# Kernel optimization log

Hardware: AMD Instinct MI355X
Metric: run time of the kernel (lower is better)

## Reference

```python
import jax, jax.numpy as jnp
import numpy as np

D_MODEL = 1024
NUM_HEADS = 16
DEPTH = D_MODEL // NUM_HEADS


def setup_inputs() -> dict:
    key = jax.random.key(0)
    ks = jax.random.split(key, 12)
    B, S = 2, 2048
    s = 0.02
    return {
        "q": jax.random.normal(ks[0], (B, S, D_MODEL), dtype=jnp.float32),
        "k": jax.random.normal(ks[1], (B, S, D_MODEL), dtype=jnp.float32),
        "v": jax.random.normal(ks[2], (B, S, D_MODEL), dtype=jnp.float32),
        "mask": jnp.ones((B, 1, 1, S), dtype=bool),  # accepted but unused, as in source
        "wq": jax.random.normal(ks[3], (D_MODEL, D_MODEL), dtype=jnp.float32) * s,
        "bq": jnp.zeros((D_MODEL,), dtype=jnp.float32),
        "wk": jax.random.normal(ks[4], (D_MODEL, D_MODEL), dtype=jnp.float32) * s,
        "bk": jnp.zeros((D_MODEL,), dtype=jnp.float32),
        "wv": jax.random.normal(ks[5], (D_MODEL, D_MODEL), dtype=jnp.float32) * s,
        "bv": jnp.zeros((D_MODEL,), dtype=jnp.float32),
        "wo": jax.random.normal(ks[6], (D_MODEL, D_MODEL), dtype=jnp.float32) * s,
        "bo": jnp.zeros((D_MODEL,), dtype=jnp.float32),
    }


def _split_heads(x, B):
    # [B, S, d_model] -> [B, H, S, depth]
    return x.reshape(B, -1, NUM_HEADS, DEPTH).transpose(0, 2, 1, 3)


def reference(q, k, v, mask, wq, bq, wk, bk, wv, bv, wo, bo):
    B = q.shape[0]
    qh = _split_heads(q @ wq + bq, B)  # [B,H,Sq,depth]
    kh = _split_heads(k @ wk + bk, B)  # [B,H,Sk,depth]
    vh = _split_heads(v @ wv + bv, B)  # [B,H,Sk,depth]
    scale = 1.0 / jnp.sqrt(jnp.asarray(DEPTH, dtype=qh.dtype))
    scores = jnp.einsum("bhqd,bhkd->bhqk", qh, kh) * scale  # [B,H,Sq,Sk]
    attn = jax.nn.softmax(scores, axis=-1)
    ctx = jnp.einsum("bhqk,bhkd->bhqd", attn, vh)  # [B,H,Sq,depth]
    concat = ctx.transpose(0, 2, 1, 3).reshape(B, -1, D_MODEL)  # [B,Sq,d_model]
    out = concat @ wo + bo
    return (out, attn)
```

## Files before the change

kernel.cpp:

```cpp
#include <hip/hip_runtime.h>
#include <hip/hip_bf16.h>
#include <cstdint>
#include <cstddef>

#define BATCH 2
#define SEQ 2048
#define NH 16
#define DH 64
#define DM 1024
#define MTOT 4096

typedef __attribute__((ext_vector_type(8))) short short8;
typedef __attribute__((ext_vector_type(4))) float f32x4;

#define MFMA16(a, b, c) __builtin_amdgcn_mfma_f32_16x16x32_bf16((a), (b), (c), 0, 0, 0)

__device__ __forceinline__ unsigned short f2bf(float f) {
  unsigned int u = __builtin_bit_cast(unsigned int, f);
  u += 0x7fffu + ((u >> 16) & 1u);
  return (unsigned short)(u >> 16);
}

__global__ __launch_bounds__(256) void cvt_x(const float* __restrict__ q,
                                             const float* __restrict__ k,
                                             const float* __restrict__ v,
                                             unsigned short* __restrict__ dst) {
  const float* srcs[3] = {q, k, v};
  const float* s = srcs[blockIdx.y];
  unsigned short* d = dst + (size_t)blockIdx.y * (MTOT * DM);
  int i = blockIdx.x * 256 + threadIdx.x;
  if (i < (MTOT * DM / 4)) {
    float4 f = ((const float4*)s)[i];
    ushort4 o;
    o.x = f2bf(f.x); o.y = f2bf(f.y); o.z = f2bf(f.z); o.w = f2bf(f.w);
    ((ushort4*)d)[i] = o;
  }
}

__global__ __launch_bounds__(256) void cvt_w(const float* __restrict__ w0,
                                             const float* __restrict__ w1,
                                             const float* __restrict__ w2,
                                             const float* __restrict__ w3,
                                             unsigned short* __restrict__ dst) {
  const float* srcs[4] = {w0, w1, w2, w3};
  const float* src = srcs[blockIdx.z];
  unsigned short* d = dst + (size_t)blockIdx.z * (DM * DM);
  __shared__ float t[32][33];
  int tx = threadIdx.x & 31, ty = threadIdx.x >> 5;
  int k0 = blockIdx.y * 32, n0 = blockIdx.x * 32;
#pragma unroll
  for (int r = 0; r < 32; r += 8) t[ty + r][tx] = src[(k0 + ty + r) * DM + n0 + tx];
  __syncthreads();
#pragma unroll
  for (int r = 0; r < 32; r += 8) d[(n0 + ty + r) * DM + k0 + tx] = f2bf(t[tx][ty + r]);
}

template <int KIND>
__global__ __launch_bounds__(256) void gemm_t64(const unsigned short* __restrict__ Abase,
                                                const unsigned short* __restrict__ Wbase,
                                                const float* __restrict__ b0,
                                                const float* __restrict__ b1,
                                                const float* __restrict__ b2,
                                                void* __restrict__ outbase) {
  const int z = (KIND == 0) ? blockIdx.z : 0;
  const unsigned short* A = Abase + (size_t)z * MTOT * DM;
  const unsigned short* Bt = Wbase + (size_t)z * DM * DM;
  const float* bias = (KIND == 1) ? b0 : (z == 0 ? b0 : (z == 1 ? b1 : b2));

  __shared__ unsigned short As[128 * 32];
  __shared__ unsigned short Bs[64 * 32];
  int tid = threadIdx.x, lane = tid & 63;
  int w = tid >> 6;
  int quad = lane >> 4, l15 = lane & 15;
  int m0 = blockIdx.x * 128, n0 = blockIdx.y * 64;
  f32x4 acc[2][4] = {};

  int r0 = tid >> 2;
  int c0 = (tid & 3) * 8;
  const uint4* ga0 = (const uint4*)(A + (size_t)(m0 + r0) * DM + c0);
  const uint4* ga1 = (const uint4*)(A + (size_t)(m0 + 64 + r0) * DM + c0);
  const uint4* gb  = (const uint4*)(Bt + (size_t)(n0 + r0) * DM + c0);

  for (int k0 = 0; k0 < DM; k0 += 32) {
    uint4 va0 = ga0[k0 >> 3];
    uint4 va1 = ga1[k0 >> 3];
    uint4 vb  = gb[k0 >> 3];
    __syncthreads();
    *(uint4*)(As + tid * 8) = va0;
    *(uint4*)(As + 2048 + tid * 8) = va1;
    *(uint4*)(Bs + tid * 8) = vb;
    __syncthreads();
    short8 af[2], bfr[4];
#pragma unroll
    for (int i = 0; i < 2; i++)
      af[i] = *(const short8*)(As + (w * 32 + i * 16 + l15) * 32 + quad * 8);
#pragma unroll
    for (int j = 0; j < 4; j++)
      bfr[j] = *(const short8*)(Bs + (j * 16 + l15) * 32 + quad * 8);
#pragma unroll
    for (int i = 0; i < 2; i++)
#pragma unroll
      for (int j = 0; j < 4; j++) acc[i][j] = MFMA16(af[i], bfr[j], acc[i][j]);
  }

  float bvals[4];
#pragma unroll
  for (int j = 0; j < 4; j++) bvals[j] = bias[n0 + j * 16 + l15];
#pragma unroll
  for (int i = 0; i < 2; i++) {
#pragma unroll
    for (int j = 0; j < 4; j++) {
#pragma unroll
      for (int r = 0; r < 4; r++) {
        int m = m0 + w * 32 + i * 16 + quad * 4 + r;
        int n = n0 + j * 16 + l15;
        float v = acc[i][j][r] + bvals[j];
        if (KIND == 1) {
          ((float*)outbase)[(size_t)m * DM + n] = v;
        } else {
          unsigned short* dq = (unsigned short*)outbase + (size_t)z * MTOT * DM;
          if (z < 2) {
            dq[(((size_t)((m >> 11) * 16 + (n >> 6)) * SEQ + (m & 2047)) * DH) + (n & 63)] = f2bf(v);
          } else {
            dq[(((size_t)((m >> 11) * 16 + (n >> 6)) * DH + (n & 63)) * SEQ) + (m & 2047)] = f2bf(v);
          }
        }
      }
    }
  }
}

__global__ __launch_bounds__(128) void attn_fused(const unsigned short* __restrict__ Qh,
                                                  const unsigned short* __restrict__ Kh,
                                                  const unsigned short* __restrict__ VhT,
                                                  float* __restrict__ attn_out,
                                                  unsigned short* __restrict__ ctx) {
  int bh = blockIdx.x;
  int q0 = blockIdx.y * 32;
  int tid = threadIdx.x, w = tid >> 6, lane = tid & 63;
  int quad = lane >> 4, l15 = lane & 15;
  int qrow = q0 + w * 16;
  const unsigned short* Qb = Qh + ((size_t)bh * SEQ + qrow) * DH;
  const unsigned short* Kb = Kh + (size_t)bh * SEQ * DH;
  const unsigned short* Vb = VhT + (size_t)bh * DH * SEQ;

  short8 aq0 = *(const short8*)(Qb + l15 * DH + quad * 8);
  short8 aq1 = *(const short8*)(Qb + l15 * DH + 32 + quad * 8);

  float part[4] = {0.f, 0.f, 0.f, 0.f};
  for (int kt = 0; kt < SEQ; kt += 32) {
    const unsigned short* kp = Kb + (size_t)(kt + l15) * DH + quad * 8;
    short8 k00 = *(const short8*)(kp);
    short8 k01 = *(const short8*)(kp + 32);
    short8 k10 = *(const short8*)(kp + 16 * DH);
    short8 k11 = *(const short8*)(kp + 16 * DH + 32);
    f32x4 s0 = {0.f, 0.f, 0.f, 0.f}, s1 = {0.f, 0.f, 0.f, 0.f};
    s0 = MFMA16(aq0, k00, s0);
    s0 = MFMA16(aq1, k01, s0);
    s1 = MFMA16(aq0, k10, s1);
    s1 = MFMA16(aq1, k11, s1);
#pragma unroll
    for (int r = 0; r < 4; r++)
      part[r] += __expf(s0[r] * 0.125f) + __expf(s1[r] * 0.125f);
  }
#pragma unroll
  for (int off = 1; off < 16; off <<= 1) {
#pragma unroll
    for (int r = 0; r < 4; r++) part[r] += __shfl_xor(part[r], off, 64);
  }
  float inv[4];
#pragma unroll
  for (int r = 0; r < 4; r++) inv[r] = 1.0f / part[r];

  __shared__ float plds[2][16 * 36];
  float* pl = &plds[w][0];
  f32x4 cacc0 = {}, cacc1 = {}, cacc2 = {}, cacc3 = {};
  float* arow = attn_out + ((size_t)bh * SEQ + qrow) * SEQ;

  for (int kt = 0; kt < SEQ; kt += 32) {
    const unsigned short* vp = Vb + (size_t)l15 * SEQ + kt + quad * 8;
    short8 bv0 = *(const short8*)(vp);
    short8 bv1 = *(const short8*)(vp + 16 * SEQ);
    short8 bv2 = *(const short8*)(vp + 32 * SEQ);
    short8 bv3 = *(const short8*)(vp + 48 * SEQ);

    const unsigned short* kp = Kb + (size_t)(kt + l15) * DH + quad * 8;
    short8 k00 = *(const short8*)(kp);
    short8 k01 = *(const short8*)(kp + 32);
    short8 k10 = *(const short8*)(kp + 16 * DH);
    short8 k11 = *(const short8*)(kp + 16 * DH + 32);
    f32x4 s0 = {0.f, 0.f, 0.f, 0.f}, s1 = {0.f, 0.f, 0.f, 0.f};
    s0 = MFMA16(aq0, k00, s0);
    s0 = MFMA16(aq1, k01, s0);
    s1 = MFMA16(aq0, k10, s1);
    s1 = MFMA16(aq1, k11, s1);
#pragma unroll
    for (int r = 0; r < 4; r++) {
      float p0 = __expf(s0[r] * 0.125f) * inv[r];
      float p1 = __expf(s1[r] * 0.125f) * inv[r];
      pl[(quad * 4 + r) * 36 + l15] = p0;
      pl[(quad * 4 + r) * 36 + 16 + l15] = p1;
    }
    {
      int rr = lane >> 3, cc = (lane & 7) * 4;
      f32x4 row0 = *(const f32x4*)(pl + rr * 36 + cc);
      f32x4 row1 = *(const f32x4*)(pl + (rr + 8) * 36 + cc);
      __builtin_nontemporal_store(row0, (f32x4*)(arow + (size_t)rr * SEQ + kt + cc));
      __builtin_nontemporal_store(row1, (f32x4*)(arow + (size_t)(rr + 8) * SEQ + kt + cc));
    }
    f32x4 pf0 = *(const f32x4*)(pl + l15 * 36 + quad * 8);
    f32x4 pf1 = *(const f32x4*)(pl + l15 * 36 + quad * 8 + 4);
    short8 pa;
    pa[0] = (short)f2bf(pf0[0]); pa[1] = (short)f2bf(pf0[1]);
    pa[2] = (short)f2bf(pf0[2]); pa[3] = (short)f2bf(pf0[3]);
    pa[4] = (short)f2bf(pf1[0]); pa[5] = (short)f2bf(pf1[1]);
    pa[6] = (short)f2bf(pf1[2]); pa[7] = (short)f2bf(pf1[3]);
    cacc0 = MFMA16(pa, bv0, cacc0);
    cacc1 = MFMA16(pa, bv1, cacc1);
    cacc2 = MFMA16(pa, bv2, cacc2);
    cacc3 = MFMA16(pa, bv3, cacc3);
  }

  int b = bh >> 4, h = bh & 15;
  f32x4 cc[4] = {cacc0, cacc1, cacc2, cacc3};
#pragma unroll
  for (int dt = 0; dt < 4; dt++) {
#pragma unroll
    for (int r = 0; r < 4; r++) {
      int m = b * SEQ + qrow + quad * 4 + r;
      int c = h * DH + dt * 16 + l15;
      ctx[(size_t)m * DM + c] = f2bf(cc[dt][r]);
    }
  }
}

extern "C" void kernel_launch(void* const* d_in, const int* in_sizes, int n_in,
                              void* d_out, int out_size, void* d_ws, size_t ws_size,
                              hipStream_t stream) {
  const float* q  = (const float*)d_in[0];
  const float* k  = (const float*)d_in[1];
  const float* v  = (const float*)d_in[2];
  const float* wq = (const float*)d_in[4];
  const float* bq = (const float*)d_in[5];
  const float* wk = (const float*)d_in[6];
  const float* bk = (const float*)d_in[7];
  const float* wv = (const float*)d_in[8];
  const float* bv = (const float*)d_in[9];
  const float* wo = (const float*)d_in[10];
  const float* bo = (const float*)d_in[11];

  char* ws = (char*)d_ws;
  unsigned short* xb  = (unsigned short*)(ws);
  unsigned short* wT  = (unsigned short*)(ws + (size_t)24 * 1024 * 1024);
  unsigned short* QH  = (unsigned short*)(ws + (size_t)32 * 1024 * 1024);
  unsigned short* KH  = (unsigned short*)(ws + (size_t)40 * 1024 * 1024);
  unsigned short* VT  = (unsigned short*)(ws + (size_t)48 * 1024 * 1024);
  unsigned short* CTX = (unsigned short*)(ws + (size_t)56 * 1024 * 1024);

  float* out_proj = (float*)d_out;
  float* attn_out = (float*)d_out + (size_t)MTOT * DM;

  cvt_x<<<dim3(MTOT * DM / 4 / 256, 3), 256, 0, stream>>>(q, k, v, xb);
  cvt_w<<<dim3(32, 32, 4), 256, 0, stream>>>(wq, wk, wv, wo, wT);

  gemm_t64<0><<<dim3(32, 16, 3), 256, 0, stream>>>(xb, wT, bq, bk, bv, QH);

  attn_fused<<<dim3(BATCH * NH, SEQ / 32), 128, 0, stream>>>(QH, KH, VT, attn_out, CTX);

  gemm_t64<1><<<dim3(32, 16), 256, 0, stream>>>(CTX, wT + (size_t)3 * DM * DM, bo, bo, bo, out_proj);
}
```

Baseline: 938.4 us.

## Split attention over key ranges, atomically accumulate fp32 context, stage V transpose stores

Splits the fused attention kernel into a row-sum pass partitioned four ways over keys and a PV pass partitioned two ways over keys. Partial context is accumulated with fp32 atomics into a zeroed buffer, and the output GEMM converts that fp32 context to bf16 while loading it. The V-transpose epilogue of the QKV GEMM now stages tiles through shared memory so it can write coalesced 16-byte stores. The aim is more blocks in flight for the attention stage; the cost is an extra memset, atomic traffic, a second read of Q and K, and a GEMM load path that now reads fp32.

```diff
diff --git a/kernel.cpp b/kernel.cpp
--- a/kernel.cpp
+++ b/kernel.cpp
@@ -9,6 +9,8 @@
 #define DH 64
 #define DM 1024
 #define MTOT 4096
+#define SPLIT1 4
+#define SPLIT2 2
 
 typedef __attribute__((ext_vector_type(8))) short short8;
 typedef __attribute__((ext_vector_type(4))) float f32x4;
@@ -56,19 +58,19 @@
 }
 
 template <int KIND>
-__global__ __launch_bounds__(256) void gemm_t64(const unsigned short* __restrict__ Abase,
+__global__ __launch_bounds__(256) void gemm_t64(const void* __restrict__ Abase,
                                                 const unsigned short* __restrict__ Wbase,
                                                 const float* __restrict__ b0,
                                                 const float* __restrict__ b1,
                                                 const float* __restrict__ b2,
                                                 void* __restrict__ outbase) {
   const int z = (KIND == 0) ? blockIdx.z : 0;
-  const unsigned short* A = Abase + (size_t)z * MTOT * DM;
   const unsigned short* Bt = Wbase + (size_t)z * DM * DM;
-  const float* bias = (KIND == 1) ? b0 : (z == 0 ? b0 : (z == 1 ? b1 : b2));
+  const float* bias = (KIND == 2) ? b0 : (z == 0 ? b0 : (z == 1 ? b1 : b2));
 
   __shared__ unsigned short As[128 * 32];
   __shared__ unsigned short Bs[64 * 32];
+  __shared__ unsigned short Es[4][32 * 32];
   int tid = threadIdx.x, lane = tid & 63;
   int w = tid >> 6;
   int quad = lane >> 4, l15 = lane & 15;
@@ -77,14 +79,31 @@
 
   int r0 = tid >> 2;
   int c0 = (tid & 3) * 8;
-  const uint4* ga0 = (const uint4*)(A + (size_t)(m0 + r0) * DM + c0);
-  const uint4* ga1 = (const uint4*)(A + (size_t)(m0 + 64 + r0) * DM + c0);
+  const unsigned short* A16 = (const unsigned short*)Abase + (size_t)z * MTOT * DM;
+  const uint4* ga0 = (const uint4*)(A16 + (size_t)(m0 + r0) * DM + c0);
+  const uint4* ga1 = (const uint4*)(A16 + (size_t)(m0 + 64 + r0) * DM + c0);
+  const float* Af = (const float*)Abase;
+  const float4* fa0 = (const float4*)(Af + (size_t)(m0 + r0) * DM + c0);
+  const float4* fa1 = (const float4*)(Af + (size_t)(m0 + 64 + r0) * DM + c0);
   const uint4* gb  = (const uint4*)(Bt + (size_t)(n0 + r0) * DM + c0);
 
   for (int k0 = 0; k0 < DM; k0 += 32) {
-    uint4 va0 = ga0[k0 >> 3];
-    uint4 va1 = ga1[k0 >> 3];
-    uint4 vb  = gb[k0 >> 3];
+    uint4 va0, va1;
+    if constexpr (KIND == 0) {
+      va0 = ga0[k0 >> 3];
+      va1 = ga1[k0 >> 3];
+    } else {
+      float4 u0 = fa0[k0 >> 2], u1 = fa0[(k0 >> 2) + 1];
+      float4 w0f = fa1[k0 >> 2], w1f = fa1[(k0 >> 2) + 1];
+      short8 p0, p1;
+      p0[0] = (short)f2bf(u0.x); p0[1] = (short)f2bf(u0.y); p0[2] = (short)f2bf(u0.z); p0[3] = (short)f2bf(u0.w);
+      p0[4] = (short)f2bf(u1.x); p0[5] = (short)f2bf(u1.y); p0[6] = (short)f2bf(u1.z); p0[7] = (short)f2bf(u1.w);
+      p1[0] = (short)f2bf(w0f.x); p1[1] = (short)f2bf(w0f.y); p1[2] = (short)f2bf(w0f.z); p1[3] = (short)f2bf(w0f.w);
+      p1[4] = (short)f2bf(w1f.x); p1[5] = (short)f2bf(w1f.y); p1[6] = (short)f2bf(w1f.z); p1[7] = (short)f2bf(w1f.w);
+      va0 = __builtin_bit_cast(uint4, p0);
+      va1 = __builtin_bit_cast(uint4, p1);
+    }
+    uint4 vb = gb[k0 >> 3];
     __syncthreads();
     *(uint4*)(As + tid * 8) = va0;
     *(uint4*)(As + 2048 + tid * 8) = va1;
@@ -106,49 +125,77 @@
   float bvals[4];
 #pragma unroll
   for (int j = 0; j < 4; j++) bvals[j] = bias[n0 + j * 16 + l15];
-#pragma unroll
-  for (int i = 0; i < 2; i++) {
-#pragma unroll
-    for (int j = 0; j < 4; j++) {
-#pragma unroll
-      for (int r = 0; r < 4; r++) {
-        int m = m0 + w * 32 + i * 16 + quad * 4 + r;
-        int n = n0 + j * 16 + l15;
-        float v = acc[i][j][r] + bvals[j];
-        if (KIND == 1) {
-          ((float*)outbase)[(size_t)m * DM + n] = v;
-        } else {
-          unsigned short* dq = (unsigned short*)outbase + (size_t)z * MTOT * DM;
-          if (z < 2) {
-            dq[(((size_t)((m >> 11) * 16 + (n >> 6)) * SEQ + (m & 2047)) * DH) + (n & 63)] = f2bf(v);
-          } else {
-            dq[(((size_t)((m >> 11) * 16 + (n >> 6)) * DH + (n & 63)) * SEQ) + (m & 2047)] = f2bf(v);
+
+  if constexpr (KIND == 2) {
+#pragma unroll
+    for (int i = 0; i < 2; i++)
+#pragma unroll
+      for (int j = 0; j < 4; j++)
+#pragma unroll
+        for (int r = 0; r < 4; r++) {
+          int m = m0 + w * 32 + i * 16 + quad * 4 + r;
+          int n = n0 + j * 16 + l15;
+          ((float*)outbase)[(size_t)m * DM + n] = acc[i][j][r] + bvals[j];
+        }
+  } else {
+    unsigned short* dq = (unsigned short*)outbase + (size_t)z * MTOT * DM;
+    if (z < 2) {
+#pragma unroll
+      for (int i = 0; i < 2; i++)
+#pragma unroll
+        for (int j = 0; j < 4; j++)
+#pragma unroll
+          for (int r = 0; r < 4; r++) {
+            int m = m0 + w * 32 + i * 16 + quad * 4 + r;
+            int n = n0 + j * 16 + l15;
+            dq[(((size_t)((m >> 11) * 16 + (n >> 6)) * SEQ + (m & 2047)) * DH) + (n & 63)] =
+                f2bf(acc[i][j][r] + bvals[j]);
           }
+    } else {
+      int bh_v = (m0 >> 11) * 16 + (n0 >> 6);
+      int s_base = (m0 & 2047) + w * 32;
+#pragma unroll
+      for (int half = 0; half < 2; half++) {
+#pragma unroll
+        for (int jj = 0; jj < 2; jj++) {
+          int j = half * 2 + jj;
+#pragma unroll
+          for (int i = 0; i < 2; i++)
+#pragma unroll
+            for (int r = 0; r < 4; r++)
+              Es[w][(jj * 16 + l15) * 32 + (i * 16 + quad * 4 + r)] = f2bf(acc[i][j][r] + bvals[j]);
+        }
+        int nl = lane >> 2;
+        int mloc = (lane & 3) * 8;
+#pragma unroll
+        for (int g = 0; g < 2; g++) {
+          int nrow = g * 16 + nl;
+          short8 val = *(const short8*)(&Es[w][nrow * 32 + mloc]);
+          *(short8*)(dq + ((size_t)(bh_v * 64 + half * 32 + nrow)) * SEQ + s_base + mloc) = val;
         }
       }
     }
   }
 }
 
-__global__ __launch_bounds__(128) void attn_fused(const unsigned short* __restrict__ Qh,
-                                                  const unsigned short* __restrict__ Kh,
-                                                  const unsigned short* __restrict__ VhT,
-                                                  float* __restrict__ attn_out,
-                                                  unsigned short* __restrict__ ctx) {
+__global__ __launch_bounds__(128) void attn_sums(const unsigned short* __restrict__ Qh,
+                                                 const unsigned short* __restrict__ Kh,
+                                                 float* __restrict__ sums) {
   int bh = blockIdx.x;
   int q0 = blockIdx.y * 32;
+  int z = blockIdx.z;
   int tid = threadIdx.x, w = tid >> 6, lane = tid & 63;
   int quad = lane >> 4, l15 = lane & 15;
   int qrow = q0 + w * 16;
   const unsigned short* Qb = Qh + ((size_t)bh * SEQ + qrow) * DH;
   const unsigned short* Kb = Kh + (size_t)bh * SEQ * DH;
-  const unsigned short* Vb = VhT + (size_t)bh * DH * SEQ;
 
   short8 aq0 = *(const short8*)(Qb + l15 * DH + quad * 8);
   short8 aq1 = *(const short8*)(Qb + l15 * DH + 32 + quad * 8);
 
   float part[4] = {0.f, 0.f, 0.f, 0.f};
-  for (int kt = 0; kt < SEQ; kt += 32) {
+  int k0 = z * (SEQ / SPLIT1);
+  for (int kt = k0; kt < k0 + SEQ / SPLIT1; kt += 32) {
     const unsigned short* kp = Kb + (size_t)(kt + l15) * DH + quad * 8;
     short8 k00 = *(const short8*)(kp);
     short8 k01 = *(const short8*)(kp + 32);
@@ -168,16 +215,46 @@
 #pragma unroll
     for (int r = 0; r < 4; r++) part[r] += __shfl_xor(part[r], off, 64);
   }
+  if (l15 == 0) {
+#pragma unroll
+    for (int r = 0; r < 4; r++)
+      sums[((size_t)bh * SEQ + qrow + quad * 4 + r) * SPLIT1 + z] = part[r];
+  }
+}
+
+__global__ __launch_bounds__(128) void attn_pv(const unsigned short* __restrict__ Qh,
+                                               const unsigned short* __restrict__ Kh,
+                                               const unsigned short* __restrict__ VhT,
+                                               const float* __restrict__ sums,
+                                               float* __restrict__ attn_out,
+                                               float* __restrict__ ctx32) {
+  int bh = blockIdx.x;
+  int q0 = blockIdx.y * 32;
+  int z = blockIdx.z;
+  int tid = threadIdx.x, w = tid >> 6, lane = tid & 63;
+  int quad = lane >> 4, l15 = lane & 15;
+  int qrow = q0 + w * 16;
+  const unsigned short* Qb = Qh + ((size_t)bh * SEQ + qrow) * DH;
+  const unsigned short* Kb = Kh + (size_t)bh * SEQ * DH;
+  const unsigned short* Vb = VhT + (size_t)bh * DH * SEQ;
+
+  short8 aq0 = *(const short8*)(Qb + l15 * DH + quad * 8);
+  short8 aq1 = *(const short8*)(Qb + l15 * DH + 32 + quad * 8);
+
   float inv[4];
 #pragma unroll
-  for (int r = 0; r < 4; r++) inv[r] = 1.0f / part[r];
+  for (int r = 0; r < 4; r++) {
+    float4 p = *(const float4*)(sums + ((size_t)bh * SEQ + qrow + quad * 4 + r) * SPLIT1);
+    inv[r] = 1.0f / (p.x + p.y + p.z + p.w);
+  }
 
   __shared__ float plds[2][16 * 36];
   float* pl = &plds[w][0];
   f32x4 cacc0 = {}, cacc1 = {}, cacc2 = {}, cacc3 = {};
   float* arow = attn_out + ((size_t)bh * SEQ + qrow) * SEQ;
 
-  for (int kt = 0; kt < SEQ; kt += 32) {
+  int koff = z * (SEQ / SPLIT2);
+  for (int kt = koff; kt < koff + SEQ / SPLIT2; kt += 32) {
     const unsigned short* vp = Vb + (size_t)l15 * SEQ + kt + quad * 8;
     short8 bv0 = *(const short8*)(vp);
     short8 bv1 = *(const short8*)(vp + 16 * SEQ);
@@ -229,7 +306,7 @@
     for (int r = 0; r < 4; r++) {
       int m = b * SEQ + qrow + quad * 4 + r;
       int c = h * DH + dt * 16 + l15;
-      ctx[(size_t)m * DM + c] = f2bf(cc[dt][r]);
+      atomicAdd(&ctx32[(size_t)m * DM + c], cc[dt][r]);
     }
   }
 }
@@ -251,11 +328,12 @@
 
   char* ws = (char*)d_ws;
   unsigned short* xb  = (unsigned short*)(ws);
+  float*          CTX32 = (float*)(ws);
+  float*          sums  = (float*)(ws + (size_t)16 * 1024 * 1024);
   unsigned short* wT  = (unsigned short*)(ws + (size_t)24 * 1024 * 1024);
   unsigned short* QH  = (unsigned short*)(ws + (size_t)32 * 1024 * 1024);
   unsigned short* KH  = (unsigned short*)(ws + (size_t)40 * 1024 * 1024);
   unsigned short* VT  = (unsigned short*)(ws + (size_t)48 * 1024 * 1024);
-  unsigned short* CTX = (unsigned short*)(ws + (size_t)56 * 1024 * 1024);
 
   float* out_proj = (float*)d_out;
   float* attn_out = (float*)d_out + (size_t)MTOT * DM;
@@ -265,7 +343,11 @@
 
   gemm_t64<0><<<dim3(32, 16, 3), 256, 0, stream>>>(xb, wT, bq, bk, bv, QH);
 
-  attn_fused<<<dim3(BATCH * NH, SEQ / 32), 128, 0, stream>>>(QH, KH, VT, attn_out, CTX);
-
-  gemm_t64<1><<<dim3(32, 16), 256, 0, stream>>>(CTX, wT + (size_t)3 * DM * DM, bo, bo, bo, out_proj);
-}
+  hipMemsetAsync(CTX32, 0, (size_t)MTOT * DM * sizeof(float), stream);
+
+  attn_sums<<<dim3(BATCH * NH, SEQ / 32, SPLIT1), 128, 0, stream>>>(QH, KH, sums);
+
+  attn_pv<<<dim3(BATCH * NH, SEQ / 32, SPLIT2), 128, 0, stream>>>(QH, KH, VT, sums, attn_out, CTX32);
+
+  gemm_t64<2><<<dim3(32, 16), 256, 0, stream>>>(CTX32, wT + (size_t)3 * DM * DM, bo, bo, bo, out_proj);
+}
```

After: 956.9 us. Within noise of the previous version (+2.0%).
